# Kernel tuning notes

Measured on AMD Instinct MI355X. Metric: run time of the kernel, lower is better.

The kernel has to match this reference:

```python
import jax, jax.numpy as jnp
import numpy as np

# RWKV6Attention config (fla): expand_k=expand_v=0.5, proj_low_rank_dim=64, gate_low_rank_dim=64
H = 2048          # hidden_size
NH = 16           # num heads
KD = H // 2       # key_dim = hidden * expand_k
VD = H // 2       # value_dim = hidden * expand_v
DK = KD // NH     # head_qk_dim = 64
DV = VD // NH     # head_v_dim = 64
RLOW = 64         # proj_low_rank_dim
GLOW = 64         # gate_low_rank_dim
EPS = 1e-5
B, T = 2, 1024


def setup_inputs() -> dict:
    key = jax.random.key(0)
    ks = jax.random.split(key, 18)

    def rn(k, shape, scale=0.02):
        return (jax.random.normal(k, shape) * scale).astype(jnp.float32)

    return {
        "x": jax.random.normal(ks[0], (B, T, H), dtype=jnp.float32),
        "mu_x": rn(ks[1], (H,), 0.5),            # LerpLinear mixing coeff
        "Wx1": rn(ks[2], (H, 5 * RLOW)),          # x_proj[0].linear (hidden -> 5*r)
        "Wx2": rn(ks[3], (H, 5, RLOW)),           # x_proj[2].weight viewed [hidden, 5, r]
        "x_bias": rn(ks[4], (5, H)),
        "Wr": rn(ks[5], (H, KD)),
        "Wk": rn(ks[6], (H, KD)),
        "Wv": rn(ks[7], (H, VD)),
        "Ww_a": rn(ks[8], (H, GLOW)),             # w_proj LoRA down
        "Ww_b": rn(ks[9], (GLOW, KD)),            # w_proj LoRA up
        "bw": rn(ks[10], (KD,)),
        "Wg_a": rn(ks[11], (H, GLOW)),            # g_proj LoRA down
        "Wg_b": rn(ks[12], (GLOW, VD)),           # g_proj LoRA up
        "bg": rn(ks[13], (VD,)),
        "bonus": rn(ks[14], (NH, DK), 0.5),       # per-head bonus u
        "ln_w": jnp.ones((DV,), jnp.float32),     # FusedLayerNormSwishGate affine
        "ln_b": jnp.zeros((DV,), jnp.float32),
        "Wo": rn(ks[15], (VD, H)),
    }


def reference(x, mu_x, Wx1, Wx2, x_bias, Wr, Wk, Wv, Ww_a, Ww_b, bw,
              Wg_a, Wg_b, bg, bonus, ln_w, ln_b, Wo):
    b, t, _ = x.shape
    # time_shift: zero-pad one step at front, drop last
    shifted = jnp.pad(x, ((0, 0), (1, 0), (0, 0)))[:, :t]
    delta = shifted - x

    # low-rank data-dependent lerp coefficients for r, w, k, v, g
    lr = jnp.tanh(((x + delta * mu_x) @ Wx1).reshape(b, t, 5, RLOW))
    mus = jnp.einsum('btnr,hnr->btnh', lr, Wx2) + x_bias  # [B,T,5,H]
    mr, mw, mk, mv, mg = (mus[:, :, i] for i in range(5))

    r = (x + delta * mr) @ Wr                                   # [B,T,KD]
    w = jnp.tanh((x + delta * mw) @ Ww_a) @ Ww_b + bw           # [B,T,KD]
    k = (x + delta * mk) @ Wk                                   # [B,T,KD]
    v = (x + delta * mv) @ Wv                                   # [B,T,VD]
    g = jnp.tanh((x + delta * mg) @ Wg_a) @ Wg_b + bg           # [B,T,VD]

    r = r.reshape(b, t, NH, DK)
    k = k.reshape(b, t, NH, DK)
    v = v.reshape(b, t, NH, DV)
    decay = jnp.exp(-jnp.exp(w.reshape(b, t, NH, DK)))          # w = -exp(w); decay = exp(w)

    # linear-attention recurrence: o_t = r_t . (S + u * k_t v_t^T); S <- decay_t * S + k_t v_t^T
    xs = (jnp.moveaxis(r, 1, 0), jnp.moveaxis(k, 1, 0),
          jnp.moveaxis(v, 1, 0), jnp.moveaxis(decay, 1, 0))
    S0 = jnp.zeros((b, NH, DK, DV), x.dtype)

    def step(S, inp):
        rt, kt, vt, dt = inp
        kv = kt[..., :, None] * vt[..., None, :]                # [B,NH,DK,DV]
        ot = jnp.einsum('bhk,bhkv->bhv', rt, S + bonus[None, :, :, None] * kv)
        S = dt[..., None] * S + kv
        return S, ot

    _, o = jax.lax.scan(step, S0, xs)                           # o: [T,B,NH,DV]
    o = jnp.moveaxis(o, 0, 1)                                   # [B,T,NH,DV]

    # per-head layernorm + swish gate
    g = g.reshape(b, t, NH, DV)
    mean = o.mean(-1, keepdims=True)
    var = o.var(-1, keepdims=True)
    on = (o - mean) * jax.lax.rsqrt(var + EPS) * ln_w + ln_b
    o = on * g * jax.nn.sigmoid(g)

    return o.reshape(b, t, VD) @ Wo
```

## Files before the change

### kernel.cpp

```cpp
#include <hip/hip_runtime.h>
#include <hip/hip_bf16.h>

#define H_    2048
#define NH_   16
#define KD_   1024
#define DK_   64
#define T_    1024
#define B_    2
#define M_    (B_*T_)
#define RL_   64
#define CC_   32
#define NC_   (T_/CC_)

typedef short bf16x8 __attribute__((ext_vector_type(8)));
typedef float f32x4  __attribute__((ext_vector_type(4)));

__device__ __forceinline__ ushort bf16r(float f) {
    union { float f; unsigned u; } v; v.f = f;
    return (ushort)((v.u + 0x7FFF + ((v.u >> 16) & 1)) >> 16);
}

__device__ __forceinline__ void gl_lds16(const void* g, void* l) {
    __builtin_amdgcn_global_load_lds((const __attribute__((address_space(1))) void*)g,
                                     (__attribute__((address_space(3))) void*)l, 16, 0, 0);
}

__device__ __forceinline__ void xcd_swz(int& bx, int& by, int& bz) {
    int gx = gridDim.x, gy = gridDim.y;
    int nwg = gx * gy * gridDim.z;
    int bid = ((int)blockIdx.z * gy + blockIdx.y) * gx + blockIdx.x;
    int swz = (bid & 7) * (nwg >> 3) + (bid >> 3);
    bx = swz % gx;
    int rem = swz / gx;
    by = rem % gy;
    bz = rem / gy;
}


__device__ __forceinline__ void conv_body(const float* __restrict__ W,
                                          ushort* __restrict__ Wt,
                                          int K, int N, int kb, int nb,
                                          float (*s)[68], int t) {
    #pragma unroll
    for (int i = 0; i < 2; ++i) {
        int q = t + i * 256;
        int k = q >> 4, c4 = (q & 15) << 2;
        *(float4*)&s[k][c4] = *(const float4*)&W[(size_t)(kb * 32 + k) * N + nb * 64 + c4];
    }
    __syncthreads();
    int g = t >> 6, c = t & 63;
    ushort o[8];
    #pragma unroll
    for (int e = 0; e < 8; ++e) o[e] = bf16r(s[g * 8 + e][c]);
    *(uint4*)&Wt[((size_t)(nb * (K >> 5) + kb)) * 2048 + t * 8] = *(uint4*)o;
}

__global__ __launch_bounds__(256) void prep_all(const float* __restrict__ x,
                                                const float* __restrict__ mu,
                                                const float* __restrict__ Wx1,
                                                const float* __restrict__ W0,
                                                const float* __restrict__ W1,
                                                const float* __restrict__ W2,
                                                const float* __restrict__ Wo,
                                                const float* __restrict__ Wx2,
                                                ushort* __restrict__ At,
                                                ushort* __restrict__ Wx1t,
                                                ushort* __restrict__ Wrt,
                                                ushort* __restrict__ Wot,
                                                ushort* __restrict__ wx2t) {
    __shared__ float s[64][68];
    int bid = blockIdx.x;
    int tid = threadIdx.x;
    if (bid < 2048) {
        int c = bid * 256 + tid;
        int bt = c >> 8, k8 = c & 255;
        int k = k8 << 3;
        int t = bt & (T_ - 1);
        const float* xp = &x[(size_t)bt * H_ + k];
        float4 xa = *(const float4*)xp;
        float4 xb = *(const float4*)(xp + 4);
        float4 sa = make_float4(0,0,0,0), sb = make_float4(0,0,0,0);
        if (t > 0) { sa = *(const float4*)(xp - H_); sb = *(const float4*)(xp - H_ + 4); }
        float4 ma = *(const float4*)&mu[k];
        float4 mb = *(const float4*)&mu[k + 4];
        ushort o[8];
        o[0] = bf16r(xa.x + (sa.x - xa.x) * ma.x);
        o[1] = bf16r(xa.y + (sa.y - xa.y) * ma.y);
        o[2] = bf16r(xa.z + (sa.z - xa.z) * ma.z);
        o[3] = bf16r(xa.w + (sa.w - xa.w) * ma.w);
        o[4] = bf16r(xb.x + (sb.x - xb.x) * mb.x);
        o[5] = bf16r(xb.y + (sb.y - xb.y) * mb.y);
        o[6] = bf16r(xb.z + (sb.z - xb.z) * mb.z);
        o[7] = bf16r(xb.w + (sb.w - xb.w) * mb.w);
        int rb = bt >> 7, kb = k8 >> 2, g = k8 & 3, r = bt & 127;
        *(uint4*)&At[(((size_t)(rb * 64 + kb)) << 12) + ((g << 7) + r) * 8] = *(uint4*)o;
        return;
    }
    bid -= 2048;
    if (bid < 320) {
        conv_body(Wx1, Wx1t, H_, 320, bid / 5, bid % 5, s, tid);
        return;
    }
    bid -= 320;
    if (bid < 3072) {
        int nb = bid & 15, kb = (bid >> 4) & 63, z = bid >> 10;
        const float* W = (z == 0) ? W0 : (z == 1) ? W1 : W2;
        conv_body(W, Wrt + (size_t)z * ((size_t)H_ * KD_), H_, KD_, kb, nb, s, tid);
        return;
    }
    bid -= 3072;
    if (bid < 1024) {
        conv_body(Wo, Wot, KD_, H_, bid >> 5, bid & 31, s, tid);
        return;
    }
    bid -= 1024;
    {
        int nb = bid & 31, z = bid >> 5;
        for (int q = tid; q < 1024; q += 256) {
            int row = q >> 4, c4 = (q & 15) << 2;
            *(float4*)&s[row][c4] = *(const float4*)&Wx2[(size_t)(nb * 64 + row) * 320 + z * 64 + c4];
        }
        __syncthreads();
        for (int q = tid; q < 512; q += 256) {
            int kb = q >> 8, i = q & 255;
            int g = i >> 6, c = i & 63;
            ushort o[8];
            #pragma unroll
            for (int e = 0; e < 8; ++e) o[e] = bf16r(s[c][kb * 32 + g * 8 + e]);
            *(uint4*)&wx2t[(((size_t)(z * 32 + nb)) * 2 + kb) * 2048 + i * 8] = *(uint4*)o;
        }
    }
}

template<int EPI, int NB>
__global__ __launch_bounds__(256) void gemm_bf16t(const ushort* __restrict__ A0,
                                                  const ushort* __restrict__ A1,
                                                  const ushort* __restrict__ A2,
                                                  const ushort* __restrict__ Bt0,
                                                  float* __restrict__ C0,
                                                  int K, int ldc) {
    __shared__ ushort Alds[2][8192];
    __shared__ ushort Blds[2][4096];
    int bx, by, bz;
    xcd_swz(bx, by, bz);
    int tid = threadIdx.x;
    int w = tid >> 6, l = tid & 63;
    int KB32 = K >> 5;
    int KB64 = K >> 6;
    int z = (NB > 1) ? bz : 0;
    const ushort* At = (NB > 1) ? (z == 0 ? A0 : z == 1 ? A1 : A2) : A0;
    const ushort* Bt = Bt0 + (size_t)z * ((size_t)H_ * KD_);
    float* C = C0 + (size_t)z * ((size_t)M_ * KD_);
    const ushort* Ag = At + (size_t)by * KB32 * 4096 + tid * 8;
    const ushort* Bg = Bt + (size_t)bx * KB32 * 2048 + tid * 8;
    int wr = (w >> 1) << 6, wc = (w & 1) << 5;
    int a_off = (((l >> 4) << 7) + wr + (l & 15)) << 3;
    int b_off = (((l >> 4) << 6) + wc + (l & 15)) << 3;
    f32x4 acc[8] = {};
    #pragma unroll
    for (int j = 0; j < 4; ++j) gl_lds16(Ag + j * 2048, &Alds[0][w * 512 + j * 2048]);
    #pragma unroll
    for (int j = 0; j < 2; ++j) gl_lds16(Bg + j * 2048, &Blds[0][w * 512 + j * 2048]);
    __syncthreads();
    for (int kt = 0; kt < KB64; ++kt) {
        int cur = kt & 1;
        if (kt + 1 < KB64) {
            Ag += 8192; Bg += 4096;
            int nxt = cur ^ 1;
            #pragma unroll
            for (int j = 0; j < 4; ++j) gl_lds16(Ag + j * 2048, &Alds[nxt][w * 512 + j * 2048]);
            #pragma unroll
            for (int j = 0; j < 2; ++j) gl_lds16(Bg + j * 2048, &Blds[nxt][w * 512 + j * 2048]);
        }
        #pragma unroll
        for (int kb2 = 0; kb2 < 2; ++kb2) {
            const ushort* Ab = &Alds[cur][kb2 * 4096 + a_off];
            const ushort* Bb = &Blds[cur][kb2 * 2048 + b_off];
            bf16x8 af0 = *(const bf16x8*)(Ab);
            bf16x8 af1 = *(const bf16x8*)(Ab + 128);
            bf16x8 af2 = *(const bf16x8*)(Ab + 256);
            bf16x8 af3 = *(const bf16x8*)(Ab + 384);
            bf16x8 bf0 = *(const bf16x8*)(Bb);
            bf16x8 bf1 = *(const bf16x8*)(Bb + 128);
            acc[0] = __builtin_amdgcn_mfma_f32_16x16x32_bf16(af0, bf0, acc[0], 0, 0, 0);
            acc[1] = __builtin_amdgcn_mfma_f32_16x16x32_bf16(af0, bf1, acc[1], 0, 0, 0);
            acc[2] = __builtin_amdgcn_mfma_f32_16x16x32_bf16(af1, bf0, acc[2], 0, 0, 0);
            acc[3] = __builtin_amdgcn_mfma_f32_16x16x32_bf16(af1, bf1, acc[3], 0, 0, 0);
            acc[4] = __builtin_amdgcn_mfma_f32_16x16x32_bf16(af2, bf0, acc[4], 0, 0, 0);
            acc[5] = __builtin_amdgcn_mfma_f32_16x16x32_bf16(af2, bf1, acc[5], 0, 0, 0);
            acc[6] = __builtin_amdgcn_mfma_f32_16x16x32_bf16(af3, bf0, acc[6], 0, 0, 0);
            acc[7] = __builtin_amdgcn_mfma_f32_16x16x32_bf16(af3, bf1, acc[7], 0, 0, 0);
        }
        __syncthreads();
    }
    int row0 = (by << 7) + wr + ((l >> 4) << 2);
    int col0 = (bx << 6) + wc + (l & 15);
    #pragma unroll
    for (int fr = 0; fr < 4; ++fr)
        #pragma unroll
        for (int fc = 0; fc < 2; ++fc) {
            f32x4 v = acc[fr * 2 + fc];
            #pragma unroll
            for (int q = 0; q < 4; ++q) {
                float o = v[q];
                if (EPI == 1) o = tanhf(o);
                C[(size_t)(row0 + fr * 16 + q) * ldc + col0 + fc * 16] = o;
            }
        }
}

__global__ __launch_bounds__(256) void gemm_bf16t_lr(const ushort* __restrict__ At,
                                                     const ushort* __restrict__ Bt,
                                                     ushort* __restrict__ lrt) {
    __shared__ ushort Alds[2][8192];
    __shared__ ushort Blds[2][4096];
    int bx, by, bz;
    xcd_swz(bx, by, bz);
    int tid = threadIdx.x;
    int w = tid >> 6, l = tid & 63;
    const int KB32 = H_ >> 5;
    const int KB64 = H_ >> 6;
    const ushort* Ag = At + (size_t)by * KB32 * 4096 + tid * 8;
    const ushort* Bg = Bt + (size_t)bx * KB32 * 2048 + tid * 8;
    int wr = (w >> 1) << 6, wc = (w & 1) << 5;
    int a_off = (((l >> 4) << 7) + wr + (l & 15)) << 3;
    int b_off = (((l >> 4) << 6) + wc + (l & 15)) << 3;
    f32x4 acc[8] = {};
    #pragma unroll
    for (int j = 0; j < 4; ++j) gl_lds16(Ag + j * 2048, &Alds[0][w * 512 + j * 2048]);
    #pragma unroll
    for (int j = 0; j < 2; ++j) gl_lds16(Bg + j * 2048, &Blds[0][w * 512 + j * 2048]);
    __syncthreads();
    for (int kt = 0; kt < KB64; ++kt) {
        int cur = kt & 1;
        if (kt + 1 < KB64) {
            Ag += 8192; Bg += 4096;
            int nxt = cur ^ 1;
            #pragma unroll
            for (int j = 0; j < 4; ++j) gl_lds16(Ag + j * 2048, &Alds[nxt][w * 512 + j * 2048]);
            #pragma unroll
            for (int j = 0; j < 2; ++j) gl_lds16(Bg + j * 2048, &Blds[nxt][w * 512 + j * 2048]);
        }
        #pragma unroll
        for (int kb2 = 0; kb2 < 2; ++kb2) {
            const ushort* Ab = &Alds[cur][kb2 * 4096 + a_off];
            const ushort* Bb = &Blds[cur][kb2 * 2048 + b_off];
            bf16x8 af0 = *(const bf16x8*)(Ab);
            bf16x8 af1 = *(const bf16x8*)(Ab + 128);
            bf16x8 af2 = *(const bf16x8*)(Ab + 256);
            bf16x8 af3 = *(const bf16x8*)(Ab + 384);
            bf16x8 bf0 = *(const bf16x8*)(Bb);
            bf16x8 bf1 = *(const bf16x8*)(Bb + 128);
            acc[0] = __builtin_amdgcn_mfma_f32_16x16x32_bf16(af0, bf0, acc[0], 0, 0, 0);
            acc[1] = __builtin_amdgcn_mfma_f32_16x16x32_bf16(af0, bf1, acc[1], 0, 0, 0);
            acc[2] = __builtin_amdgcn_mfma_f32_16x16x32_bf16(af1, bf0, acc[2], 0, 0, 0);
            acc[3] = __builtin_amdgcn_mfma_f32_16x16x32_bf16(af1, bf1, acc[3], 0, 0, 0);
            acc[4] = __builtin_amdgcn_mfma_f32_16x16x32_bf16(af2, bf0, acc[4], 0, 0, 0);
            acc[5] = __builtin_amdgcn_mfma_f32_16x16x32_bf16(af2, bf1, acc[5], 0, 0, 0);
            acc[6] = __builtin_amdgcn_mfma_f32_16x16x32_bf16(af3, bf0, acc[6], 0, 0, 0);
            acc[7] = __builtin_amdgcn_mfma_f32_16x16x32_bf16(af3, bf1, acc[7], 0, 0, 0);
        }
        __syncthreads();
    }
    int rloc0 = wr + ((l >> 4) << 2);
    size_t tbase = ((size_t)(by * 5 + bx)) * 8192;
    #pragma unroll
    for (int fr = 0; fr < 4; ++fr)
        #pragma unroll
        for (int fc = 0; fc < 2; ++fc) {
            f32x4 v = acc[fr * 2 + fc];
            int c = wc + fc * 16 + (l & 15);
            int kb2 = c >> 5, g = (c >> 3) & 3, e = c & 7;
            #pragma unroll
            for (int q = 0; q < 4; ++q) {
                int r = rloc0 + fr * 16 + q;
                lrt[tbase + (size_t)kb2 * 4096 + ((g << 7) + r) * 8 + e] = bf16r(tanhf(v[q]));
            }
        }
}

__global__ __launch_bounds__(256) void musgemm_mfma(const ushort* __restrict__ lrt,
                                                    const ushort* __restrict__ wx2t,
                                                    const float* __restrict__ x,
                                                    const float* __restrict__ xbias,
                                                    ushort* __restrict__ xmt_r,
                                                    float*  __restrict__ xm_w,
                                                    ushort* __restrict__ xmt_k,
                                                    ushort* __restrict__ xmt_v,
                                                    float*  __restrict__ xm_g) {
    __shared__ ushort Alds[8192];
    __shared__ ushort Blds[4096];
    int tid = threadIdx.x;
    int w = tid >> 6, l = tid & 63;
    int z = blockIdx.z;
    const ushort* Ag = lrt + ((size_t)(blockIdx.y * 5 + z)) * 8192 + tid * 8;
    const ushort* Bg = wx2t + ((size_t)(z * 32 + blockIdx.x)) * 4096 + tid * 8;
    gl_lds16(Ag,        &Alds[w * 512]);
    gl_lds16(Ag + 2048, &Alds[w * 512 + 2048]);
    gl_lds16(Ag + 4096, &Alds[w * 512 + 4096]);
    gl_lds16(Ag + 6144, &Alds[w * 512 + 6144]);
    gl_lds16(Bg,        &Blds[w * 512]);
    gl_lds16(Bg + 2048, &Blds[w * 512 + 2048]);
    int wr = (w >> 1) << 6, wc = (w & 1) << 5;
    int a_off = (((l >> 4) << 7) + wr + (l & 15)) << 3;
    int b_off = (((l >> 4) << 6) + wc + (l & 15)) << 3;
    f32x4 acc[8] = {};
    __syncthreads();
    #pragma unroll
    for (int kb = 0; kb < 2; ++kb) {
        const ushort* Ab = &Alds[kb * 4096 + a_off];
        const ushort* Bb = &Blds[kb * 2048 + b_off];
        bf16x8 af0 = *(const bf16x8*)(Ab);
        bf16x8 af1 = *(const bf16x8*)(Ab + 128);
        bf16x8 af2 = *(const bf16x8*)(Ab + 256);
        bf16x8 af3 = *(const bf16x8*)(Ab + 384);
        bf16x8 bf0 = *(const bf16x8*)(Bb);
        bf16x8 bf1 = *(const bf16x8*)(Bb + 128);
        acc[0] = __builtin_amdgcn_mfma_f32_16x16x32_bf16(af0, bf0, acc[0], 0, 0, 0);
        acc[1] = __builtin_amdgcn_mfma_f32_16x16x32_bf16(af0, bf1, acc[1], 0, 0, 0);
        acc[2] = __builtin_amdgcn_mfma_f32_16x16x32_bf16(af1, bf0, acc[2], 0, 0, 0);
        acc[3] = __builtin_amdgcn_mfma_f32_16x16x32_bf16(af1, bf1, acc[3], 0, 0, 0);
        acc[4] = __builtin_amdgcn_mfma_f32_16x16x32_bf16(af2, bf0, acc[4], 0, 0, 0);
        acc[5] = __builtin_amdgcn_mfma_f32_16x16x32_bf16(af2, bf1, acc[5], 0, 0, 0);
        acc[6] = __builtin_amdgcn_mfma_f32_16x16x32_bf16(af3, bf0, acc[6], 0, 0, 0);
        acc[7] = __builtin_amdgcn_mfma_f32_16x16x32_bf16(af3, bf1, acc[7], 0, 0, 0);
    }
    int row0 = (blockIdx.y << 7) + wr + ((l >> 4) << 2);
    int col0 = (blockIdx.x << 6) + wc + (l & 15);
    #pragma unroll
    for (int fr = 0; fr < 4; ++fr)
        #pragma unroll
        for (int fc = 0; fc < 2; ++fc) {
            f32x4 v = acc[fr * 2 + fc];
            int h = col0 + fc * 16;
            float bias = xbias[z * H_ + h];
            #pragma unroll
            for (int q = 0; q < 4; ++q) {
                int r = row0 + fr * 16 + q;
                int t = r & (T_ - 1);
                const float* xp = &x[(size_t)r * H_ + h];
                float xv = *xp;
                float sh = (t > 0) ? *(xp - H_) : 0.f;
                float o = xv + (sh - xv) * (v[q] + bias);
                if (z == 0 || z == 2 || z == 3) {
                    ushort* dst = (z == 0) ? xmt_r : (z == 2) ? xmt_k : xmt_v;
                    int rb = r >> 7, kb = h >> 5, g = (h >> 3) & 3;
                    dst[(((size_t)(rb * 64 + kb)) << 12) + ((g << 7) + (r & 127)) * 8 + (h & 7)] = bf16r(o);
                } else {
                    float* dst = (z == 1) ? xm_w : xm_g;
                    dst[(size_t)r * H_ + h] = o;
                }
            }
        }
}

__global__ __launch_bounds__(256) void gemm_f32_up2(const float* __restrict__ hidw,
                                                    const float* __restrict__ hidg,
                                                    const float* __restrict__ Wwb,
                                                    const float* __restrict__ Wgb,
                                                    const float* __restrict__ bw,
                                                    const float* __restrict__ bg,
                                                    float* __restrict__ db,
                                                    float* __restrict__ gb) {
    __shared__ float As[16][68];
    __shared__ float Bs[16][68];
    int z = blockIdx.z;
    const float* A = z ? hidg : hidw;
    const float* W = z ? Wgb : Wwb;
    const float* bias = z ? bg : bw;
    float* C = z ? gb : db;
    int tid = threadIdx.x;
    int tx = tid & 15, ty = tid >> 4;
    int row0 = blockIdx.y * 64, col0 = blockIdx.x * 64;
    int am = tid >> 2, ak = (tid & 3) << 2;
    int bk = tid >> 4, bn = (tid & 15) << 2;
    float acc[4][4] = {};
    float4 av = *(const float4*)&A[(size_t)(row0 + am) * 64 + ak];
    float4 bv = *(const float4*)&W[(size_t)bk * KD_ + col0 + bn];
    for (int k0 = 0; k0 < 64; k0 += 16) {
        __syncthreads();
        As[ak + 0][am] = av.x; As[ak + 1][am] = av.y;
        As[ak + 2][am] = av.z; As[ak + 3][am] = av.w;
        *(float4*)&Bs[bk][bn] = bv;
        __syncthreads();
        if (k0 + 16 < 64) {
            av = *(const float4*)&A[(size_t)(row0 + am) * 64 + k0 + 16 + ak];
            bv = *(const float4*)&W[(size_t)(k0 + 16 + bk) * KD_ + col0 + bn];
        }
        #pragma unroll
        for (int kk = 0; kk < 16; ++kk) {
            float4 a = *(const float4*)&As[kk][ty << 2];
            float4 b = *(const float4*)&Bs[kk][tx << 2];
            float aa[4] = {a.x, a.y, a.z, a.w};
            float bb[4] = {b.x, b.y, b.z, b.w};
            #pragma unroll
            for (int i = 0; i < 4; ++i)
                #pragma unroll
                for (int j = 0; j < 4; ++j)
                    acc[i][j] = fmaf(aa[i], bb[j], acc[i][j]);
        }
    }
    #pragma unroll
    for (int i = 0; i < 4; ++i) {
        int r = row0 + (ty << 2) + i;
        #pragma unroll
        for (int j = 0; j < 4; ++j) {
            int c = col0 + (tx << 2) + j;
            float v = acc[i][j] + bias[c];
            if (z == 0) v = -expf(v);
            C[(size_t)r * KD_ + c] = v;
        }
    }
}

__global__ __launch_bounds__(256) void gemm_f32_splitk2(const float* __restrict__ Aw,
                                                        const float* __restrict__ Ag2,
                                                        const float* __restrict__ Wwa,
                                                        const float* __restrict__ Wga,
                                                        float* __restrict__ partw,
                                                        float* __restrict__ partg) {
    __shared__ float As[16][68];
    __shared__ float Bs[16][68];
    int z = blockIdx.z;
    const float* A = z ? Ag2 : Aw;
    const float* W = z ? Wga : Wwa;
    float* part = z ? partg : partw;
    int tid = threadIdx.x;
    int tx = tid & 15, ty = tid >> 4;
    int row0 = blockIdx.y * 64;
    int kbase = blockIdx.x * 256;
    int am = tid >> 2, ak = (tid & 3) << 2;
    int bk = tid >> 4, bn = (tid & 15) << 2;
    float acc[4][4] = {};
    float4 av = *(const float4*)&A[(size_t)(row0 + am) * H_ + kbase + ak];
    float4 bv = *(const float4*)&W[(size_t)(kbase + bk) * 64 + bn];
    for (int k0 = 0; k0 < 256; k0 += 16) {
        __syncthreads();
        As[ak + 0][am] = av.x; As[ak + 1][am] = av.y;
        As[ak + 2][am] = av.z; As[ak + 3][am] = av.w;
        *(float4*)&Bs[bk][bn] = bv;
        __syncthreads();
        if (k0 + 16 < 256) {
            av = *(const float4*)&A[(size_t)(row0 + am) * H_ + kbase + k0 + 16 + ak];
            bv = *(const float4*)&W[(size_t)(kbase + k0 + 16 + bk) * 64 + bn];
        }
        #pragma unroll
        for (int kk = 0; kk < 16; ++kk) {
            float4 a = *(const float4*)&As[kk][ty << 2];
            float4 b = *(const float4*)&Bs[kk][tx << 2];
            float aa[4] = {a.x, a.y, a.z, a.w};
            float bb[4] = {b.x, b.y, b.z, b.w};
            #pragma unroll
            for (int i = 0; i < 4; ++i)
                #pragma unroll
                for (int j = 0; j < 4; ++j)
                    acc[i][j] = fmaf(aa[i], bb[j], acc[i][j]);
        }
    }
    float* pc = part + (size_t)blockIdx.x * (M_ * 64);
    #pragma unroll
    for (int i = 0; i < 4; ++i) {
        int r = row0 + (ty << 2) + i;
        #pragma unroll
        for (int j = 0; j < 4; ++j)
            pc[(size_t)r * 64 + (tx << 2) + j] = acc[i][j];
    }
}

__global__ __launch_bounds__(256) void reduce_tanh2(const float* __restrict__ partw,
                                                    const float* __restrict__ partg,
                                                    float* __restrict__ hidw,
                                                    float* __restrict__ hidg) {
    int z = blockIdx.y;
    const float4* p = (const float4*)(z ? partg : partw);
    float* hid = z ? hidg : hidw;
    int i = blockIdx.x * 256 + threadIdx.x;
    float4 s = p[i];
    #pragma unroll
    for (int kc = 1; kc < 8; ++kc) {
        float4 v = p[i + kc * 32768];
        s.x += v.x; s.y += v.y; s.z += v.z; s.w += v.w;
    }
    s.x = tanhf(s.x); s.y = tanhf(s.y); s.z = tanhf(s.z); s.w = tanhf(s.w);
    ((float4*)hid)[i] = s;
}

__global__ __launch_bounds__(512) void scan_chunkA(const float* r, const float* k,
                                                   const float* v, const float* ld,
                                                   const float* u,
                                                   float* rt, float* ointra,
                                                   float* Bc, float* Dc) {
    __shared__ float sR[CC_][68], sK[CC_][68], sV[CC_][68], sW[CC_][68];
    __shared__ float wc[CC_ + 1][64];
    __shared__ float sA[CC_][36];
    __shared__ float diag[CC_];
    __shared__ float sU[64];
    int bid = blockIdx.x;
    int bh = bid >> 5, c = bid & (NC_ - 1);
    int b = bh >> 4, h = bh & 15;
    int tid = threadIdx.x;
    size_t base = ((size_t)(b * T_ + c * CC_)) * KD_ + h * 64;

    {
        int row = tid >> 4, col4 = (tid & 15) << 2;
        size_t gi = base + (size_t)row * KD_ + col4;
        *(float4*)&sR[row][col4] = *(const float4*)&r[gi];
        *(float4*)&sK[row][col4] = *(const float4*)&k[gi];
        *(float4*)&sV[row][col4] = *(const float4*)&v[gi];
        *(float4*)&sW[row][col4] = *(const float4*)&ld[gi];
    }
    if (tid < 64) sU[tid] = u[h * 64 + tid];
    __syncthreads();

    if (tid < 64) {
        float acc = 0.f;
        wc[0][tid] = 0.f;
        #pragma unroll
        for (int s = 0; s < CC_; ++s) { acc += sW[s][tid]; wc[s + 1][tid] = acc; }
    }
    {
        int tau = tid >> 4, g = tid & 15;
        float p = 0.f;
        #pragma unroll
        for (int q = 0; q < 4; ++q) {
            int i = g * 4 + q;
            p += sR[tau][i] * sU[i] * sK[tau][i];
        }
        p += __shfl_xor(p, 1, 64); p += __shfl_xor(p, 2, 64);
        p += __shfl_xor(p, 4, 64); p += __shfl_xor(p, 8, 64);
        if (g == 0) diag[tau] = p;
    }
    __syncthreads();

    for (int q = tid; q < CC_ * 64; q += 512) {
        int s = q >> 6, i = q & 63;
        float wcs  = wc[s][i];
        float wcs1 = wc[s + 1][i];
        float wcc  = wc[CC_][i];
        float rt_ = sR[s][i] * expf(wcs);
        float kt_ = sK[s][i] * expf(-wcs1);
        float bb  = sK[s][i] * expf(wcc - wcs1);
        sR[s][i] = rt_;
        sW[s][i] = kt_;
        sK[s][i] = bb;
        rt[base + (size_t)s * KD_ + i] = rt_;
    }
    if (tid < 64) Dc[(size_t)bid * 64 + tid] = expf(wc[CC_][tid]);
    __syncthreads();

    {
        int tau = tid >> 4, s0 = (tid & 15) * 2;
        float a0 = 0, a1 = 0;
        for (int i0 = 0; i0 < 64; i0 += 4) {
            int i = (i0 + ((tid & 15) << 2)) & 63;
            float4 rr  = *(const float4*)&sR[tau][i];
            float4 k0v = *(const float4*)&sW[s0 + 0][i];
            float4 k1v = *(const float4*)&sW[s0 + 1][i];
            a0 += rr.x * k0v.x + rr.y * k0v.y + rr.z * k0v.z + rr.w * k0v.w;
            a1 += rr.x * k1v.x + rr.y * k1v.y + rr.z * k1v.z + rr.w * k1v.w;
        }
        sA[tau][s0 + 0] = (s0 + 0 < tau) ? a0 : ((s0 + 0 == tau) ? diag[tau] : 0.f);
        sA[tau][s0 + 1] = (s0 + 1 < tau) ? a1 : ((s0 + 1 == tau) ? diag[tau] : 0.f);
    }
    __syncthreads();

    {
        int tau = tid >> 4, j0 = (tid & 15) * 4;
        float o_[4] __attribute__((aligned(16))) = {};
        for (int s = 0; s < CC_; ++s) {
            float a = sA[tau][s];
            float4 vv = *(const float4*)&sV[s][j0];
            o_[0] += a * vv.x; o_[1] += a * vv.y;
            o_[2] += a * vv.z; o_[3] += a * vv.w;
        }
        size_t ob = base + (size_t)tau * KD_ + j0;
        *(float4*)&ointra[ob] = *(float4*)&o_[0];
    }
    {
        int i = tid >> 3, j0 = (tid & 7) * 8;
        float bacc[8] __attribute__((aligned(16))) = {};
        for (int s = 0; s < CC_; ++s) {
            float bi = sK[s][i];
            float4 v0 = *(const float4*)&sV[s][j0];
            float4 v1 = *(const float4*)&sV[s][j0 + 4];
            bacc[0] += bi * v0.x; bacc[1] += bi * v0.y;
            bacc[2] += bi * v0.z; bacc[3] += bi * v0.w;
            bacc[4] += bi * v1.x; bacc[5] += bi * v1.y;
            bacc[6] += bi * v1.z; bacc[7] += bi * v1.w;
        }
        size_t bb = ((size_t)bid << 12) + i * 64 + j0;
        *(float4*)&Bc[bb + 0] = *(float4*)&bacc[0];
        *(float4*)&Bc[bb + 4] = *(float4*)&bacc[4];
    }
}

__global__ __launch_bounds__(256) void scan_chunkB(float* BS, const float* __restrict__ Dc) {
    int g = blockIdx.x * 256 + threadIdx.x;
    int bh = g >> 12, ij = g & 4095, i = ij >> 6;
    float S = 0.f;
    size_t base = ((size_t)bh << 17) + ij;
    float bv = BS[base];
    float d  = Dc[(size_t)(bh * NC_) * 64 + i];
    for (int c = 0; c < NC_; ++c) {
        size_t idx = base + ((size_t)c << 12);
        float bv2 = 0.f, d2 = 0.f;
        if (c + 1 < NC_) {
            bv2 = BS[idx + 4096];
            d2  = Dc[(size_t)(bh * NC_ + c + 1) * 64 + i];
        }
        BS[idx] = S;
        S = d * S + bv;
        bv = bv2; d = d2;
    }
}

__global__ __launch_bounds__(512) void scan_chunkC_ln(const float* __restrict__ rt,
                                                      const float* __restrict__ BS,
                                                      const float* __restrict__ oi,
                                                      const float* __restrict__ gb,
                                                      const float* __restrict__ lw,
                                                      const float* __restrict__ lb,
                                                      ushort* __restrict__ outt) {
    __shared__ float sS[64][64];
    __shared__ float sRt[CC_][68];
    int bid = blockIdx.x;
    int bh = bid >> 5, c = bid & (NC_ - 1);
    int b = bh >> 4, h = bh & 15;
    int tid = threadIdx.x;
    size_t sbase = ((size_t)bid) << 12;
    for (int q = tid; q < 1024; q += 512)
        *(float4*)&sS[q >> 4][(q & 15) << 2] = *(const float4*)&BS[sbase + (q << 2)];
    size_t base = ((size_t)(b * T_ + c * CC_)) * KD_ + h * 64;
    {
        int row = tid >> 4, col4 = (tid & 15) << 2;
        *(float4*)&sRt[row][col4] = *(const float4*)&rt[base + (size_t)row * KD_ + col4];
    }
    __syncthreads();
    int tau = tid >> 4, j0 = (tid & 15) * 4;
    size_t obase = base + (size_t)tau * KD_ + j0;
    float acc[4] __attribute__((aligned(16)));
    *(float4*)&acc[0] = *(const float4*)&oi[obase];
    for (int i = 0; i < 64; ++i) {
        float a = sRt[tau][i];
        float4 vv = *(const float4*)&sS[i][j0];
        acc[0] += a * vv.x; acc[1] += a * vv.y;
        acc[2] += a * vv.z; acc[3] += a * vv.w;
    }
    float s = acc[0] + acc[1] + acc[2] + acc[3];
    s += __shfl_xor(s, 1, 64); s += __shfl_xor(s, 2, 64);
    s += __shfl_xor(s, 4, 64); s += __shfl_xor(s, 8, 64);
    float mean = s * (1.f / 64.f);
    float s2 = 0.f;
    #pragma unroll
    for (int q = 0; q < 4; ++q) { float dx = acc[q] - mean; s2 += dx * dx; }
    s2 += __shfl_xor(s2, 1, 64); s2 += __shfl_xor(s2, 2, 64);
    s2 += __shfl_xor(s2, 4, 64); s2 += __shfl_xor(s2, 8, 64);
    float inv = rsqrtf(s2 * (1.f / 64.f) + 1e-5f);
    float4 lwv = *(const float4*)&lw[j0];
    float4 lbv = *(const float4*)&lb[j0];
    float4 gv  = *(const float4*)&gb[obase];
    float lww[4] = {lwv.x, lwv.y, lwv.z, lwv.w};
    float lbb[4] = {lbv.x, lbv.y, lbv.z, lbv.w};
    float gvv[4] = {gv.x, gv.y, gv.z, gv.w};
    ushort o4[4];
    #pragma unroll
    for (int q = 0; q < 4; ++q) {
        float on = (acc[q] - mean) * inv * lww[q] + lbb[q];
        float g = gvv[q];
        o4[q] = bf16r(on * g / (1.f + expf(-g)));
    }
    int mrow = b * T_ + c * CC_ + tau;
    int col  = h * 64 + j0;
    int rb2 = mrow >> 7, kb2 = col >> 5, gg = (col >> 3) & 3;
    *(ushort4*)&outt[(((size_t)(rb2 * 32 + kb2)) << 12) + ((gg << 7) + (mrow & 127)) * 8 + (col & 7)] = *(ushort4*)o4;
}

extern "C" void kernel_launch(void* const* d_in, const int* in_sizes, int n_in,
                              void* d_out, int out_size, void* d_ws, size_t ws_size,
                              hipStream_t stream) {
    const float* x     = (const float*)d_in[0];
    const float* mu_x  = (const float*)d_in[1];
    const float* Wx1   = (const float*)d_in[2];
    const float* Wx2   = (const float*)d_in[3];
    const float* xbias = (const float*)d_in[4];
    const float* Wr    = (const float*)d_in[5];
    const float* Wk    = (const float*)d_in[6];
    const float* Wv    = (const float*)d_in[7];
    const float* Ww_a  = (const float*)d_in[8];
    const float* Ww_b  = (const float*)d_in[9];
    const float* bw    = (const float*)d_in[10];
    const float* Wg_a  = (const float*)d_in[11];
    const float* Wg_b  = (const float*)d_in[12];
    const float* bg    = (const float*)d_in[13];
    const float* bonus = (const float*)d_in[14];
    const float* ln_w  = (const float*)d_in[15];
    const float* ln_b  = (const float*)d_in[16];
    const float* Wo    = (const float*)d_in[17];
    float* out = (float*)d_out;

    float* ws   = (float*)d_ws;
    float* xm   = ws;
    float* lr   = xm   + (size_t)M_ * H_;
    float* hidw = lr   + (size_t)M_ * 320;
    float* hidg = hidw + (size_t)M_ * 64;
    float* rb_  = hidg + (size_t)M_ * 64;
    float* kb_  = rb_  + (size_t)M_ * KD_;
    float* vb_  = kb_  + (size_t)M_ * KD_;
    float* db_  = vb_  + (size_t)M_ * KD_;
    float* gb_  = db_  + (size_t)M_ * KD_;
    float* ob_  = gb_  + (size_t)M_ * KD_;
    float* BS   = ob_  + (size_t)M_ * KD_;
    float* Dc   = BS   + (size_t)1024 * 4096;
    float* wend = Dc + (size_t)1024 * 64;
    ushort* xmt_r = (ushort*)xm;
    ushort* xmt_k = (ushort*)(xm + (size_t)M_ * H_ / 2);
    ushort* xmt_v = (ushort*)(BS + 1310720);
    float*  xm_w  = rb_;
    float*  xm_g  = vb_;
    float*  partw = BS;
    float*  partg = gb_;
    ushort* gt    = (ushort*)xm;
    ushort* lrt   = (ushort*)lr;
    ushort* wx2t  = lrt + 655360;
    ushort* Wx1t  = (ushort*)wend;
    ushort* Wrt   = Wx1t + (size_t)H_ * 320;
    ushort* Wkt   = Wrt  + (size_t)H_ * KD_;
    ushort* Wvt   = Wkt  + (size_t)H_ * KD_;
    ushort* Wot   = Wvt  + (size_t)H_ * KD_;

    dim3 blk(256);

    prep_all<<<6624, blk, 0, stream>>>(x, mu_x, Wx1, Wr, Wk, Wv, Wo, Wx2,
                                       (ushort*)xm, Wx1t, Wrt, Wot, wx2t);

    gemm_bf16t_lr<<<dim3(5, M_ / 128), blk, 0, stream>>>((ushort*)xm, Wx1t, lrt);

    musgemm_mfma<<<dim3(H_ / 64, M_ / 128, 5), blk, 0, stream>>>(lrt, wx2t, x, xbias,
                                                                 xmt_r, xm_w, xmt_k, xmt_v, xm_g);

    gemm_f32_splitk2<<<dim3(8, M_ / 64, 2), blk, 0, stream>>>(xm_w, xm_g, Ww_a, Wg_a,
                                                              partw, partg);
    reduce_tanh2<<<dim3(128, 2), blk, 0, stream>>>(partw, partg, hidw, hidg);

    gemm_f32_up2<<<dim3(KD_ / 64, M_ / 64, 2), blk, 0, stream>>>(hidw, hidg, Ww_b, Wg_b,
                                                                 bw, bg, db_, gb_);

    gemm_bf16t<0, 3><<<dim3(KD_ / 64, M_ / 128, 3), blk, 0, stream>>>(xmt_r, xmt_k, xmt_v,
                                                                      Wrt, rb_, H_, KD_);

    scan_chunkA<<<B_ * NH_ * NC_, dim3(512), 0, stream>>>(rb_, kb_, vb_, db_, bonus,
                                                          rb_ , ob_, BS, Dc);
    scan_chunkB<<<(B_ * NH_ * 4096) / 256, blk, 0, stream>>>(BS, Dc);
    scan_chunkC_ln<<<B_ * NH_ * NC_, dim3(512), 0, stream>>>(rb_, BS, ob_, gb_, ln_w, ln_b, gt);

    gemm_bf16t<0, 1><<<dim3(H_ / 64, M_ / 128), blk, 0, stream>>>(gt, nullptr, nullptr,
                                                                  Wot, out, KD_, H_);
}
```

Measured before the change: 228.0 us.

## Fuse r/k/v bf16 GEMM with LoRA-down split-K GEMM into one launch

```diff
diff --git a/kernel.cpp b/kernel.cpp
--- a/kernel.cpp
+++ b/kernel.cpp
@@ -132,25 +132,20 @@
     }
 }
 
-template<int EPI, int NB>
-__global__ __launch_bounds__(256) void gemm_bf16t(const ushort* __restrict__ A0,
-                                                  const ushort* __restrict__ A1,
-                                                  const ushort* __restrict__ A2,
-                                                  const ushort* __restrict__ Bt0,
-                                                  float* __restrict__ C0,
+template<int EPI>
+__global__ __launch_bounds__(256) void gemm_bf16t(const ushort* __restrict__ At,
+                                                  const ushort* __restrict__ Bt,
+                                                  float* __restrict__ C,
                                                   int K, int ldc) {
     __shared__ ushort Alds[2][8192];
     __shared__ ushort Blds[2][4096];
     int bx, by, bz;
     xcd_swz(bx, by, bz);
+    (void)bz;
     int tid = threadIdx.x;
     int w = tid >> 6, l = tid & 63;
     int KB32 = K >> 5;
     int KB64 = K >> 6;
-    int z = (NB > 1) ? bz : 0;
-    const ushort* At = (NB > 1) ? (z == 0 ? A0 : z == 1 ? A1 : A2) : A0;
-    const ushort* Bt = Bt0 + (size_t)z * ((size_t)H_ * KD_);
-    float* C = C0 + (size_t)z * ((size_t)M_ * KD_);
     const ushort* Ag = At + (size_t)by * KB32 * 4096 + tid * 8;
     const ushort* Bg = Bt + (size_t)bx * KB32 * 2048 + tid * 8;
     int wr = (w >> 1) << 6, wc = (w & 1) << 5;
@@ -209,6 +204,138 @@
         }
 }
 
+__global__ __launch_bounds__(256) void gemm_rkv_splitk(const ushort* __restrict__ A0,
+                                                       const ushort* __restrict__ A1,
+                                                       const ushort* __restrict__ A2,
+                                                       const ushort* __restrict__ Bt0,
+                                                       float* __restrict__ C0,
+                                                       const float* __restrict__ Aw,
+                                                       const float* __restrict__ Ag2,
+                                                       const float* __restrict__ Wwa,
+                                                       const float* __restrict__ Wga,
+                                                       float* __restrict__ partw,
+                                                       float* __restrict__ partg) {
+    __shared__ ushort smem[24576];
+    int p = blockIdx.x;
+    int tid = threadIdx.x;
+    if (p < 768) {
+        ushort (*Alds)[8192] = (ushort(*)[8192])smem;
+        ushort (*Blds)[4096] = (ushort(*)[4096])(smem + 16384);
+        int swz = (p & 7) * 96 + (p >> 3);
+        int bx = swz & 15;
+        int rem = swz >> 4;
+        int by = rem & 15;
+        int bz = rem >> 4;
+        int w = tid >> 6, l = tid & 63;
+        const int KB32 = H_ >> 5, KB64 = H_ >> 6;
+        const ushort* At = (bz == 0) ? A0 : (bz == 1) ? A1 : A2;
+        const ushort* Bt = Bt0 + (size_t)bz * ((size_t)H_ * KD_);
+        float* C = C0 + (size_t)bz * ((size_t)M_ * KD_);
+        const ushort* Ag = At + (size_t)by * KB32 * 4096 + tid * 8;
+        const ushort* Bg = Bt + (size_t)bx * KB32 * 2048 + tid * 8;
+        int wr = (w >> 1) << 6, wc = (w & 1) << 5;
+        int a_off = (((l >> 4) << 7) + wr + (l & 15)) << 3;
+        int b_off = (((l >> 4) << 6) + wc + (l & 15)) << 3;
+        f32x4 acc[8] = {};
+        #pragma unroll
+        for (int j = 0; j < 4; ++j) gl_lds16(Ag + j * 2048, &Alds[0][w * 512 + j * 2048]);
+        #pragma unroll
+        for (int j = 0; j < 2; ++j) gl_lds16(Bg + j * 2048, &Blds[0][w * 512 + j * 2048]);
+        __syncthreads();
+        for (int kt = 0; kt < KB64; ++kt) {
+            int cur = kt & 1;
+            if (kt + 1 < KB64) {
+                Ag += 8192; Bg += 4096;
+                int nxt = cur ^ 1;
+                #pragma unroll
+                for (int j = 0; j < 4; ++j) gl_lds16(Ag + j * 2048, &Alds[nxt][w * 512 + j * 2048]);
+                #pragma unroll
+                for (int j = 0; j < 2; ++j) gl_lds16(Bg + j * 2048, &Blds[nxt][w * 512 + j * 2048]);
+            }
+            #pragma unroll
+            for (int kb2 = 0; kb2 < 2; ++kb2) {
+                const ushort* Ab = &Alds[cur][kb2 * 4096 + a_off];
+                const ushort* Bb = &Blds[cur][kb2 * 2048 + b_off];
+                bf16x8 af0 = *(const bf16x8*)(Ab);
+                bf16x8 af1 = *(const bf16x8*)(Ab + 128);
+                bf16x8 af2 = *(const bf16x8*)(Ab + 256);
+                bf16x8 af3 = *(const bf16x8*)(Ab + 384);
+                bf16x8 bf0 = *(const bf16x8*)(Bb);
+                bf16x8 bf1 = *(const bf16x8*)(Bb + 128);
+                acc[0] = __builtin_amdgcn_mfma_f32_16x16x32_bf16(af0, bf0, acc[0], 0, 0, 0);
+                acc[1] = __builtin_amdgcn_mfma_f32_16x16x32_bf16(af0, bf1, acc[1], 0, 0, 0);
+                acc[2] = __builtin_amdgcn_mfma_f32_16x16x32_bf16(af1, bf0, acc[2], 0, 0, 0);
+                acc[3] = __builtin_amdgcn_mfma_f32_16x16x32_bf16(af1, bf1, acc[3], 0, 0, 0);
+                acc[4] = __builtin_amdgcn_mfma_f32_16x16x32_bf16(af2, bf0, acc[4], 0, 0, 0);
+                acc[5] = __builtin_amdgcn_mfma_f32_16x16x32_bf16(af2, bf1, acc[5], 0, 0, 0);
+                acc[6] = __builtin_amdgcn_mfma_f32_16x16x32_bf16(af3, bf0, acc[6], 0, 0, 0);
+                acc[7] = __builtin_amdgcn_mfma_f32_16x16x32_bf16(af3, bf1, acc[7], 0, 0, 0);
+            }
+            __syncthreads();
+        }
+        int row0 = (by << 7) + wr + ((l >> 4) << 2);
+        int col0 = (bx << 6) + wc + (l & 15);
+        #pragma unroll
+        for (int fr = 0; fr < 4; ++fr)
+            #pragma unroll
+            for (int fc = 0; fc < 2; ++fc) {
+                f32x4 v = acc[fr * 2 + fc];
+                #pragma unroll
+                for (int q = 0; q < 4; ++q)
+                    C[(size_t)(row0 + fr * 16 + q) * KD_ + col0 + fc * 16] = v[q];
+            }
+        return;
+    }
+    {
+        int p768 = p - 768;
+        int kc = p768 & 7, ry = (p768 >> 3) & 31, z = p768 >> 8;
+        float (*As)[68] = (float(*)[68])smem;
+        float (*Bs)[68] = (float(*)[68])(smem + 2176);
+        const float* A = z ? Ag2 : Aw;
+        const float* W = z ? Wga : Wwa;
+        float* part = z ? partg : partw;
+        int tx = tid & 15, ty = tid >> 4;
+        int row0 = ry * 64;
+        int kbase = kc * 256;
+        int am = tid >> 2, ak = (tid & 3) << 2;
+        int bk = tid >> 4, bn = (tid & 15) << 2;
+        float acc[4][4] = {};
+        float4 av = *(const float4*)&A[(size_t)(row0 + am) * H_ + kbase + ak];
+        float4 bv = *(const float4*)&W[(size_t)(kbase + bk) * 64 + bn];
+        for (int k0 = 0; k0 < 256; k0 += 16) {
+            __syncthreads();
+            As[ak + 0][am] = av.x; As[ak + 1][am] = av.y;
+            As[ak + 2][am] = av.z; As[ak + 3][am] = av.w;
+            *(float4*)&Bs[bk][bn] = bv;
+            __syncthreads();
+            if (k0 + 16 < 256) {
+                av = *(const float4*)&A[(size_t)(row0 + am) * H_ + kbase + k0 + 16 + ak];
+                bv = *(const float4*)&W[(size_t)(kbase + k0 + 16 + bk) * 64 + bn];
+            }
+            #pragma unroll
+            for (int kk = 0; kk < 16; ++kk) {
+                float4 a = *(const float4*)&As[kk][ty << 2];
+                float4 b = *(const float4*)&Bs[kk][tx << 2];
+                float aa[4] = {a.x, a.y, a.z, a.w};
+                float bb[4] = {b.x, b.y, b.z, b.w};
+                #pragma unroll
+                for (int i = 0; i < 4; ++i)
+                    #pragma unroll
+                    for (int j = 0; j < 4; ++j)
+                        acc[i][j] = fmaf(aa[i], bb[j], acc[i][j]);
+            }
+        }
+        float* pc = part + (size_t)kc * (M_ * 64);
+        #pragma unroll
+        for (int i = 0; i < 4; ++i) {
+            int r = row0 + (ty << 2) + i;
+            #pragma unroll
+            for (int j = 0; j < 4; ++j)
+                pc[(size_t)r * 64 + (tx << 2) + j] = acc[i][j];
+        }
+    }
+}
+
 __global__ __launch_bounds__(256) void gemm_bf16t_lr(const ushort* __restrict__ At,
                                                      const ushort* __restrict__ Bt,
                                                      ushort* __restrict__ lrt) {
@@ -216,6 +343,7 @@
     __shared__ ushort Blds[2][4096];
     int bx, by, bz;
     xcd_swz(bx, by, bz);
+    (void)bz;
     int tid = threadIdx.x;
     int w = tid >> 6, l = tid & 63;
     const int KB32 = H_ >> 5;
@@ -413,60 +541,6 @@
     }
 }
 
-__global__ __launch_bounds__(256) void gemm_f32_splitk2(const float* __restrict__ Aw,
-                                                        const float* __restrict__ Ag2,
-                                                        const float* __restrict__ Wwa,
-                                                        const float* __restrict__ Wga,
-                                                        float* __restrict__ partw,
-                                                        float* __restrict__ partg) {
-    __shared__ float As[16][68];
-    __shared__ float Bs[16][68];
-    int z = blockIdx.z;
-    const float* A = z ? Ag2 : Aw;
-    const float* W = z ? Wga : Wwa;
-    float* part = z ? partg : partw;
-    int tid = threadIdx.x;
-    int tx = tid & 15, ty = tid >> 4;
-    int row0 = blockIdx.y * 64;
-    int kbase = blockIdx.x * 256;
-    int am = tid >> 2, ak = (tid & 3) << 2;
-    int bk = tid >> 4, bn = (tid & 15) << 2;
-    float acc[4][4] = {};
-    float4 av = *(const float4*)&A[(size_t)(row0 + am) * H_ + kbase + ak];
-    float4 bv = *(const float4*)&W[(size_t)(kbase + bk) * 64 + bn];
-    for (int k0 = 0; k0 < 256; k0 += 16) {
-        __syncthreads();
-        As[ak + 0][am] = av.x; As[ak + 1][am] = av.y;
-        As[ak + 2][am] = av.z; As[ak + 3][am] = av.w;
-        *(float4*)&Bs[bk][bn] = bv;
-        __syncthreads();
-        if (k0 + 16 < 256) {
-            av = *(const float4*)&A[(size_t)(row0 + am) * H_ + kbase + k0 + 16 + ak];
-            bv = *(const float4*)&W[(size_t)(kbase + k0 + 16 + bk) * 64 + bn];
-        }
-        #pragma unroll
-        for (int kk = 0; kk < 16; ++kk) {
-            float4 a = *(const float4*)&As[kk][ty << 2];
-            float4 b = *(const float4*)&Bs[kk][tx << 2];
-            float aa[4] = {a.x, a.y, a.z, a.w};
-            float bb[4] = {b.x, b.y, b.z, b.w};
-            #pragma unroll
-            for (int i = 0; i < 4; ++i)
-                #pragma unroll
-                for (int j = 0; j < 4; ++j)
-                    acc[i][j] = fmaf(aa[i], bb[j], acc[i][j]);
-        }
-    }
-    float* pc = part + (size_t)blockIdx.x * (M_ * 64);
-    #pragma unroll
-    for (int i = 0; i < 4; ++i) {
-        int r = row0 + (ty << 2) + i;
-        #pragma unroll
-        for (int j = 0; j < 4; ++j)
-            pc[(size_t)r * 64 + (tx << 2) + j] = acc[i][j];
-    }
-}
-
 __global__ __launch_bounds__(256) void reduce_tanh2(const float* __restrict__ partw,
                                                     const float* __restrict__ partg,
                                                     float* __restrict__ hidw,
@@ -715,8 +789,6 @@
     ushort* xmt_r = (ushort*)xm;
     ushort* xmt_k = (ushort*)(xm + (size_t)M_ * H_ / 2);
     ushort* xmt_v = (ushort*)(BS + 1310720);
-    float*  xm_w  = rb_;
-    float*  xm_g  = vb_;
     float*  partw = BS;
     float*  partg = gb_;
     ushort* gt    = (ushort*)xm;
@@ -727,6 +799,8 @@
     ushort* Wkt   = Wrt  + (size_t)H_ * KD_;
     ushort* Wvt   = Wkt  + (size_t)H_ * KD_;
     ushort* Wot   = Wvt  + (size_t)H_ * KD_;
+    float*  xm_w  = (float*)(Wot + (size_t)KD_ * H_);
+    float*  xm_g  = xm_w + (size_t)M_ * H_;
 
     dim3 blk(256);
 
@@ -738,21 +812,17 @@
     musgemm_mfma<<<dim3(H_ / 64, M_ / 128, 5), blk, 0, stream>>>(lrt, wx2t, x, xbias,
                                                                  xmt_r, xm_w, xmt_k, xmt_v, xm_g);
 
-    gemm_f32_splitk2<<<dim3(8, M_ / 64, 2), blk, 0, stream>>>(xm_w, xm_g, Ww_a, Wg_a,
-                                                              partw, partg);
+    gemm_rkv_splitk<<<1280, blk, 0, stream>>>(xmt_r, xmt_k, xmt_v, Wrt, rb_,
+                                              xm_w, xm_g, Ww_a, Wg_a, partw, partg);
+
     reduce_tanh2<<<dim3(128, 2), blk, 0, stream>>>(partw, partg, hidw, hidg);
-
     gemm_f32_up2<<<dim3(KD_ / 64, M_ / 64, 2), blk, 0, stream>>>(hidw, hidg, Ww_b, Wg_b,
                                                                  bw, bg, db_, gb_);
-
-    gemm_bf16t<0, 3><<<dim3(KD_ / 64, M_ / 128, 3), blk, 0, stream>>>(xmt_r, xmt_k, xmt_v,
-                                                                      Wrt, rb_, H_, KD_);
 
     scan_chunkA<<<B_ * NH_ * NC_, dim3(512), 0, stream>>>(rb_, kb_, vb_, db_, bonus,
                                                           rb_ , ob_, BS, Dc);
     scan_chunkB<<<(B_ * NH_ * 4096) / 256, blk, 0, stream>>>(BS, Dc);
     scan_chunkC_ln<<<B_ * NH_ * NC_, dim3(512), 0, stream>>>(rb_, BS, ob_, gb_, ln_w, ln_b, gt);
 
-    gemm_bf16t<0, 1><<<dim3(H_ / 64, M_ / 128), blk, 0, stream>>>(gt, nullptr, nullptr,
-                                                                  Wot, out, KD_, H_);
-}
+    gemm_bf16t<0><<<dim3(H_ / 64, M_ / 128), blk, 0, stream>>>(gt, Wot, out, KD_, H_);
+}
```

After: 224.6 us, median of 3. About the same (-1.5%).
